# Performance work log

Measured on AMD Instinct MI355X. Metric: run time of the kernel, lower is better.

Reference implementation:

```python
import jax, jax.numpy as jnp
import numpy as np

COORD_W, EDGE_W, COUNT_W, REG_W, CONTRA_W = 1.0, 2.0, 0.1, 0.001, 0.1
MARGIN = 1.0


def setup_inputs() -> dict:
    key = jax.random.key(0)
    ks = jax.random.split(key, 6)
    B, N, D, C = 16, 1024, 128, 2
    return {
        "predicted_coords": jax.random.normal(ks[0], (B, N, C), jnp.float32),
        "points": jax.random.normal(ks[1], (B, N, C), jnp.float32),
        "adjacency_logits": jax.random.normal(ks[2], (B, N, N), jnp.float32),
        "adjacency": jax.random.bernoulli(ks[3], 0.1, (B, N, N)).astype(jnp.float32),
        "node_masks": jnp.ones((B, N), jnp.float32),  # all nodes valid -> n_actual = N
        "predicted_count": jax.random.normal(ks[4], (B, 1), jnp.float32),
        "node_features": jax.random.normal(ks[5], (B, N, D), jnp.float32),
    }


def _bce_with_logits(logits, targets):
    # mean-reduced, numerically stable (matches F.binary_cross_entropy_with_logits)
    return jnp.mean(jnp.maximum(logits, 0.0) - logits * targets
                    + jnp.log1p(jnp.exp(-jnp.abs(logits))))


def _smooth_l1(pred, target):
    d = jnp.abs(pred - target)
    return jnp.mean(jnp.where(d < 1.0, 0.5 * d * d, d - 0.5))


def _contrastive_sample(features, adj):
    # features: [N, D], adj: [N, N]. torch.cdist pairwise euclidean via gram trick.
    nrm = jnp.sum(features * features, axis=-1)              # [N]
    sq = jnp.maximum(nrm[:, None] + nrm[None, :]
                     - 2.0 * (features @ features.T), 0.0)   # [N, N] squared dists
    n = features.shape[0]
    eye = jnp.eye(n, dtype=bool)
    pos_mask = adj > 0.5
    neg_mask = (adj <= 0.5) & (~eye)
    # positive term: mean of distances**2 over positive pairs == mean squared dist
    pos = jnp.sum(jnp.where(pos_mask, sq, 0.0)) / jnp.maximum(jnp.sum(pos_mask), 1)
    dist = jnp.sqrt(jnp.maximum(sq, 1e-12))
    hinge = jnp.square(jax.nn.relu(MARGIN - dist))
    neg = jnp.sum(jnp.where(neg_mask, hinge, 0.0)) / jnp.maximum(jnp.sum(neg_mask), 1)
    return pos + neg


def reference(predicted_coords, points, adjacency_logits, adjacency,
              node_masks, predicted_count, node_features):
    # node_masks are all ones, so the per-sample [:n_actual] slicing is the
    # full tensor; per-sample MSE/BCE means averaged over batch equal global means.
    coord_loss = jnp.mean(jnp.square(predicted_coords - points))
    edge_loss = _bce_with_logits(adjacency_logits, adjacency)
    actual_counts = jnp.sum(node_masks, axis=1)              # [B]
    count_loss = _smooth_l1(predicted_count[:, 0], actual_counts)
    reg_loss = jnp.mean(jnp.square(node_features))
    # contrastive path uses targets['adjacency'] (no predicted_adjacency key)
    contra_loss = jnp.mean(jax.vmap(_contrastive_sample)(node_features, adjacency))
    total = (COORD_W * coord_loss + EDGE_W * edge_loss + COUNT_W * count_loss
             + REG_W * reg_loss + CONTRA_W * contra_loss)
    return total, coord_loss, edge_loss, count_loss, reg_loss, contra_loss
```

## Files before the change

kernel.cpp:

```cpp
#include <hip/hip_runtime.h>
#include <hip/hip_bf16.h>

#define NN 1024
#define DD 128
#define TS 64
#define PITCH 136

#define WS_COORD 0
#define WS_REG   1
#define WS_BCE   2
#define WS_POSN  3
#define WS_POSC  19
#define WS_NEGS  35
#define WS_PDIAG 51
#define WS_CROSS 67
#define WS_CNT   83
#define WS_NORM  112

typedef __bf16 bf16_t;
typedef bf16_t bf16x8 __attribute__((ext_vector_type(8)));
typedef float  f32x4  __attribute__((ext_vector_type(4)));

__device__ __forceinline__ void gload16(const void* g, void* l) {
  __builtin_amdgcn_global_load_lds(
      (const __attribute__((address_space(1))) uint32_t*)g,
      (__attribute__((address_space(3))) uint32_t*)l,
      16, 0, 0);
}

__global__ __launch_bounds__(256) void prep(
    const float* __restrict__ feat, const float* __restrict__ pcoord,
    const float* __restrict__ pts,  const float* __restrict__ masks,
    float* __restrict__ ws) {
  __shared__ float red[4][3];
  const int bx = blockIdx.x;
  const int b = bx >> 3, slab = bx & 7;
  const int t = threadIdx.x, lane = t & 63, w = t >> 6;
  const int sub = lane >> 4, lq = lane & 15;
  const float* fb = feat + (size_t)b * NN * DD;

  float reg = 0.f;
  #pragma unroll
  for (int it = 0; it < 8; ++it) {
    const int node = slab * 128 + it * 16 + w * 4 + sub;
    const float4* src = (const float4*)(fb + (size_t)node * DD) + lq * 2;
    float4 u = src[0], v = src[1];
    float s = u.x*u.x + u.y*u.y + u.z*u.z + u.w*u.w
            + v.x*v.x + v.y*v.y + v.z*v.z + v.w*v.w;
    s += __shfl_xor(s, 1); s += __shfl_xor(s, 2);
    s += __shfl_xor(s, 4); s += __shfl_xor(s, 8);
    if (lq == 0) { ws[WS_NORM + b * NN + node] = s; reg += s; }
  }
  const int ci = bx * 256 + t;
  const float d = pcoord[ci] - pts[ci];
  float coord = d * d;
  float cnt = (t < 128) ? masks[b * NN + slab * 128 + t] : 0.f;

  #pragma unroll
  for (int o = 32; o; o >>= 1) {
    coord += __shfl_xor(coord, o);
    reg   += __shfl_xor(reg, o);
    cnt   += __shfl_xor(cnt, o);
  }
  if (lane == 0) { red[w][0] = coord; red[w][1] = reg; red[w][2] = cnt; }
  __syncthreads();
  if (t == 0) {
    float c = 0.f, r = 0.f, n = 0.f;
    for (int i = 0; i < 4; ++i) { c += red[i][0]; r += red[i][1]; n += red[i][2]; }
    atomicAdd(&ws[WS_COORD], c);
    atomicAdd(&ws[WS_REG], r);
    atomicAdd(&ws[WS_CNT + b], n);
  }
}

__global__ __launch_bounds__(256, 4) void lds_stream(
    const float* __restrict__ logits, const float* __restrict__ adj,
    float* __restrict__ ws) {
  __shared__ __align__(16) float4 sL[2][512];
  __shared__ __align__(16) float4 sA[2][512];
  __shared__ float red[4][4];
  const int bx = blockIdx.x;
  const int b = bx >> 6, rb = bx & 63;
  const int t = threadIdx.x, lane = t & 63, w = t >> 6;
  const float4* Lg = (const float4*)logits + (size_t)b * 262144 + (size_t)rb * 4096;
  const float4* Ag = (const float4*)adj    + (size_t)b * 262144 + (size_t)rb * 4096;
  const float* nrm = ws + WS_NORM + b * NN;

  const float4 nj = ((const float4*)nrm)[t];
  float ni[16];
  #pragma unroll
  for (int k = 0; k < 16; ++k) ni[k] = nrm[rb * 16 + k];

#define STAGE(s) do {                                              \
    gload16(Lg + (s) * 512 + t,       &sL[(s) & 1][t]);            \
    gload16(Lg + (s) * 512 + 256 + t, &sL[(s) & 1][t + 256]);      \
    gload16(Ag + (s) * 512 + t,       &sA[(s) & 1][t]);            \
    gload16(Ag + (s) * 512 + 256 + t, &sA[(s) & 1][t + 256]);      \
  } while (0)

#define ELEM4(L, A, nv, grow) do {                                            \
    bce += fmaxf(L.x, 0.f) - L.x * A.x + __logf(1.f + __expf(-fabsf(L.x)));   \
    bce += fmaxf(L.y, 0.f) - L.y * A.y + __logf(1.f + __expf(-fabsf(L.y)));   \
    bce += fmaxf(L.z, 0.f) - L.z * A.z + __logf(1.f + __expf(-fabsf(L.z)));   \
    bce += fmaxf(L.w, 0.f) - L.w * A.w + __logf(1.f + __expf(-fabsf(L.w)));   \
    const float px = (A.x > 0.5f) ? 1.f : 0.f;                                \
    const float py = (A.y > 0.5f) ? 1.f : 0.f;                                \
    const float pz = (A.z > 0.5f) ? 1.f : 0.f;                                \
    const float pw = (A.w > 0.5f) ? 1.f : 0.f;                                \
    posc += px + py + pz + pw;                                                \
    posn += px * (nv + nj.x) + py * (nv + nj.y)                               \
          + pz * (nv + nj.z) + pw * (nv + nj.w);                              \
    if (((grow) >> 2) == t) {                                                 \
      const int e = (grow) & 3;                                               \
      const float av = (e == 0) ? A.x : (e == 1) ? A.y : (e == 2) ? A.z : A.w;\
      pdiag += (av > 0.5f) ? 1.f : 0.f;                                       \
    } } while (0)

  float bce = 0.f, posc = 0.f, posn = 0.f, pdiag = 0.f;
  STAGE(0);
  #pragma unroll
  for (int s = 0; s < 8; ++s) {
    if (s < 7) STAGE(s + 1);
    const float4 L0 = sL[s & 1][t];
    const float4 A0 = sA[s & 1][t];
    const float4 L1 = sL[s & 1][t + 256];
    const float4 A1 = sA[s & 1][t + 256];
    const int g0 = rb * 16 + s * 2;
    ELEM4(L0, A0, ni[s * 2], g0);
    ELEM4(L1, A1, ni[s * 2 + 1], g0 + 1);
  }
#undef STAGE
#undef ELEM4

  #pragma unroll
  for (int o = 32; o; o >>= 1) {
    bce   += __shfl_xor(bce, o);
    posc  += __shfl_xor(posc, o);
    posn  += __shfl_xor(posn, o);
    pdiag += __shfl_xor(pdiag, o);
  }
  if (lane == 0) {
    red[w][0] = bce; red[w][1] = posc; red[w][2] = posn; red[w][3] = pdiag;
  }
  __syncthreads();
  if (t == 0) {
    float s0 = 0.f, s1 = 0.f, s2 = 0.f, s3 = 0.f;
    for (int i = 0; i < 4; ++i) {
      s0 += red[i][0]; s1 += red[i][1]; s2 += red[i][2]; s3 += red[i][3];
    }
    atomicAdd(&ws[WS_BCE], s0);
    atomicAdd(&ws[WS_POSC + b], s1);
    atomicAdd(&ws[WS_POSN + b], s2);
    atomicAdd(&ws[WS_PDIAG + b], s3);
  }
}

__global__ __launch_bounds__(256, 4) void gram_tiles(
    const float* __restrict__ adj, const float* __restrict__ feat,
    float* __restrict__ ws) {
  __shared__ __align__(16) char smem[2 * TS * PITCH * sizeof(bf16_t)];
  __shared__ float red[4][2];
  bf16_t* lsA = (bf16_t*)smem;
  bf16_t* lsB = (bf16_t*)(smem + TS * PITCH * sizeof(bf16_t));

  const int gid = blockIdx.x;
  const int bm = ((gid & 7) << 9) | (gid >> 3);
  const int b = bm >> 8, tid = bm & 255;
  const int ti = (tid >> 4) << 6, tj = (tid & 15) << 6;
  const int t = threadIdx.x, lane = t & 63, wave = t >> 6;
  const int lrow = lane & 15, quad = lane >> 4;
  const float* fb = feat + (size_t)b * NN * DD;
  const float* nrm = ws + WS_NORM + b * NN;

  const int rbase = wave * 16 + quad * 4;
  const int grow0 = ti + rbase;
  const float* ap = adj + (size_t)b * NN * NN + (size_t)grow0 * NN + (tj + lrow);
  float Af[4][4];
  #pragma unroll
  for (int r = 0; r < 4; ++r)
    #pragma unroll
    for (int fc = 0; fc < 4; ++fc)
      Af[fc][r] = ap[(size_t)r * NN + fc * 16];
  const float4 niv = *(const float4*)(nrm + grow0);
  float njv[4];
  #pragma unroll
  for (int fc = 0; fc < 4; ++fc) njv[fc] = nrm[tj + fc * 16 + lrow];
  __builtin_amdgcn_sched_barrier(0);

  #pragma unroll
  for (int it = 0; it < 8; ++it) {
    const int cid = it * 256 + t;
    const int tile = cid >> 10;
    const int sub = cid & 1023;
    const int row = sub >> 4;
    const int c8 = sub & 15;
    const float* src = fb + (size_t)((tile ? tj : ti) + row) * DD + c8 * 8;
    const float4 u = *(const float4*)src;
    const float4 v = *(const float4*)(src + 4);
    bf16x8 pk;
    pk[0]=(bf16_t)u.x; pk[1]=(bf16_t)u.y; pk[2]=(bf16_t)u.z; pk[3]=(bf16_t)u.w;
    pk[4]=(bf16_t)v.x; pk[5]=(bf16_t)v.y; pk[6]=(bf16_t)v.z; pk[7]=(bf16_t)v.w;
    *(bf16x8*)((tile ? lsB : lsA) + row * PITCH + c8 * 8) = pk;
  }
  __syncthreads();

  f32x4 acc[4];
  #pragma unroll
  for (int fc = 0; fc < 4; ++fc) acc[fc] = (f32x4){0.f, 0.f, 0.f, 0.f};
  #pragma unroll
  for (int k0 = 0; k0 < DD; k0 += 32) {
    const int kc = k0 + quad * 8;
    const bf16x8 aF = *(const bf16x8*)&lsA[(wave * 16 + lrow) * PITCH + kc];
    #pragma unroll
    for (int fc = 0; fc < 4; ++fc) {
      const bf16x8 bF = *(const bf16x8*)&lsB[(fc * 16 + lrow) * PITCH + kc];
      acc[fc] = __builtin_amdgcn_mfma_f32_16x16x32_bf16(aF, bF, acc[fc], 0, 0, 0);
    }
  }

  float cross = 0.f, negs = 0.f;
  #pragma unroll
  for (int fc = 0; fc < 4; ++fc) {
    const int gcol = tj + fc * 16 + lrow;
    #pragma unroll
    for (int r = 0; r < 4; ++r) {
      const float a = Af[fc][r];
      const float g = acc[fc][r];
      if (a > 0.5f) {
        cross += g;
      } else {
        const int grow = grow0 + r;
        const float ni = (r == 0) ? niv.x : (r == 1) ? niv.y : (r == 2) ? niv.z : niv.w;
        const float sq = ni + njv[fc] - 2.f * g;
        if (sq < 1.f && grow != gcol) {
          const float dd = sqrtf(fmaxf(sq, 1e-12f));
          const float h = 1.f - dd;
          negs += h * h;
        }
      }
    }
  }
  #pragma unroll
  for (int o = 32; o; o >>= 1) {
    cross += __shfl_xor(cross, o);
    negs  += __shfl_xor(negs, o);
  }
  if (lane == 0) { red[wave][0] = cross; red[wave][1] = negs; }
  __syncthreads();
  if (t == 0) {
    float s0 = 0.f, s1 = 0.f;
    for (int i = 0; i < 4; ++i) { s0 += red[i][0]; s1 += red[i][1]; }
    atomicAdd(&ws[WS_CROSS + b], s0);
    atomicAdd(&ws[WS_NEGS + b], s1);
  }
}

__global__ void finalize(const float* __restrict__ ws, const float* __restrict__ pcount,
                         float* __restrict__ out) {
  if (threadIdx.x != 0 || blockIdx.x != 0) return;
  const float coord = ws[WS_COORD] / 32768.f;
  const float reg   = ws[WS_REG] / 2097152.f;
  const float edge  = ws[WS_BCE] / 16777216.f;
  float cntl = 0.f, contra = 0.f;
  for (int b = 0; b < 16; ++b) {
    const float d = fabsf(pcount[b] - ws[WS_CNT + b]);
    cntl += (d < 1.f) ? 0.5f * d * d : d - 0.5f;
    const float posc = ws[WS_POSC + b];
    const float pos = (ws[WS_POSN + b] - 2.f * ws[WS_CROSS + b]) / fmaxf(posc, 1.f);
    const float negc = 1024.f * 1024.f - 1024.f - (posc - ws[WS_PDIAG + b]);
    const float neg = ws[WS_NEGS + b] / fmaxf(negc, 1.f);
    contra += pos + neg;
  }
  cntl *= (1.f / 16.f);
  contra *= (1.f / 16.f);
  const float total = coord + 2.f * edge + 0.1f * cntl + 0.001f * reg + 0.1f * contra;
  out[0] = total; out[1] = coord; out[2] = edge;
  out[3] = cntl;  out[4] = reg;   out[5] = contra;
}

extern "C" void kernel_launch(void* const* d_in, const int* in_sizes, int n_in,
                              void* d_out, int out_size, void* d_ws, size_t ws_size,
                              hipStream_t stream) {
  (void)in_sizes; (void)n_in; (void)out_size; (void)ws_size;
  const float* pcoord = (const float*)d_in[0];
  const float* pts    = (const float*)d_in[1];
  const float* logits = (const float*)d_in[2];
  const float* adj    = (const float*)d_in[3];
  const float* masks  = (const float*)d_in[4];
  const float* pcount = (const float*)d_in[5];
  const float* nf     = (const float*)d_in[6];
  float* ws  = (float*)d_ws;
  float* out = (float*)d_out;

  hipMemsetAsync(ws, 0, WS_NORM * sizeof(float), stream);
  prep<<<128, 256, 0, stream>>>(nf, pcoord, pts, masks, ws);
  lds_stream<<<1024, 256, 0, stream>>>(logits, adj, ws);
  gram_tiles<<<4096, 256, 0, stream>>>(adj, nf, ws);
  finalize<<<1, 64, 0, stream>>>(ws, pcount, out);
}
```

Baseline: 242.7 us.

## Restructure gram pass into row bands and interleave stream blocks across batches

The gram kernel now has each block own a 16-row band of one batch. It caches that band's adjacency rows in LDS as bf16 and loops over eight 128-column chunks, converting features to bf16 per chunk, so each block makes one contiguous adjacency pass instead of 64x64 tiles with strided loads. The BCE streaming kernel remaps blocks so each block covers two rows across eight batches, with per-batch partial sums and more atomics per block, which spreads concurrent blocks over different batches. The cost is that the column features are re-read and re-converted by all 64 bands, there are more syncthreads per block, and the block count drops to 1024 blocks of 512 threads, which may reduce latency hiding.

```diff
diff --git a/kernel.cpp b/kernel.cpp
--- a/kernel.cpp
+++ b/kernel.cpp
@@ -3,8 +3,6 @@
 
 #define NN 1024
 #define DD 128
-#define TS 64
-#define PITCH 136
 
 #define WS_COORD 0
 #define WS_REG   1
@@ -18,6 +16,7 @@
 #define WS_NORM  112
 
 typedef __bf16 bf16_t;
+typedef bf16_t bf16x4 __attribute__((ext_vector_type(4)));
 typedef bf16_t bf16x8 __attribute__((ext_vector_type(8)));
 typedef float  f32x4  __attribute__((ext_vector_type(4)));
 
@@ -78,27 +77,28 @@
     float* __restrict__ ws) {
   __shared__ __align__(16) float4 sL[2][512];
   __shared__ __align__(16) float4 sA[2][512];
-  __shared__ float red[4][4];
+  __shared__ float red[4][25];
   const int bx = blockIdx.x;
-  const int b = bx >> 6, rb = bx & 63;
+  const int hi = bx >> 9;
+  const int r0 = (bx & 511) * 2;
   const int t = threadIdx.x, lane = t & 63, w = t >> 6;
-  const float4* Lg = (const float4*)logits + (size_t)b * 262144 + (size_t)rb * 4096;
-  const float4* Ag = (const float4*)adj    + (size_t)b * 262144 + (size_t)rb * 4096;
-  const float* nrm = ws + WS_NORM + b * NN;
-
-  const float4 nj = ((const float4*)nrm)[t];
-  float ni[16];
-  #pragma unroll
-  for (int k = 0; k < 16; ++k) ni[k] = nrm[rb * 16 + k];
-
-#define STAGE(s) do {                                              \
-    gload16(Lg + (s) * 512 + t,       &sL[(s) & 1][t]);            \
-    gload16(Lg + (s) * 512 + 256 + t, &sL[(s) & 1][t + 256]);      \
-    gload16(Ag + (s) * 512 + t,       &sA[(s) & 1][t]);            \
-    gload16(Ag + (s) * 512 + 256 + t, &sA[(s) & 1][t + 256]);      \
+  const float4* Lg = (const float4*)logits;
+  const float4* Ag = (const float4*)adj;
+
+  float bce = 0.f;
+  float pc[8], pn[8], pd[8];
+  #pragma unroll
+  for (int s = 0; s < 8; ++s) { pc[s] = 0.f; pn[s] = 0.f; pd[s] = 0.f; }
+
+#define STAGE(s) do {                                                  \
+    const size_t c4 = (size_t)((s) * 1024 + bx) * 512;                 \
+    gload16(Lg + c4 + t,       &sL[(s) & 1][t]);                       \
+    gload16(Lg + c4 + 256 + t, &sL[(s) & 1][t + 256]);                 \
+    gload16(Ag + c4 + t,       &sA[(s) & 1][t]);                       \
+    gload16(Ag + c4 + 256 + t, &sA[(s) & 1][t + 256]);                 \
   } while (0)
 
-#define ELEM4(L, A, nv, grow) do {                                            \
+#define ELEM4(L, A, nv, grow, S) do {                                         \
     bce += fmaxf(L.x, 0.f) - L.x * A.x + __logf(1.f + __expf(-fabsf(L.x)));   \
     bce += fmaxf(L.y, 0.f) - L.y * A.y + __logf(1.f + __expf(-fabsf(L.y)));   \
     bce += fmaxf(L.z, 0.f) - L.z * A.z + __logf(1.f + __expf(-fabsf(L.z)));   \
@@ -107,149 +107,160 @@
     const float py = (A.y > 0.5f) ? 1.f : 0.f;                                \
     const float pz = (A.z > 0.5f) ? 1.f : 0.f;                                \
     const float pw = (A.w > 0.5f) ? 1.f : 0.f;                                \
-    posc += px + py + pz + pw;                                                \
-    posn += px * (nv + nj.x) + py * (nv + nj.y)                               \
-          + pz * (nv + nj.z) + pw * (nv + nj.w);                              \
+    pc[S] += px + py + pz + pw;                                               \
+    pn[S] += px * (nv + nj.x) + py * (nv + nj.y)                              \
+           + pz * (nv + nj.z) + pw * (nv + nj.w);                             \
     if (((grow) >> 2) == t) {                                                 \
       const int e = (grow) & 3;                                               \
       const float av = (e == 0) ? A.x : (e == 1) ? A.y : (e == 2) ? A.z : A.w;\
-      pdiag += (av > 0.5f) ? 1.f : 0.f;                                       \
+      pd[S] += (av > 0.5f) ? 1.f : 0.f;                                       \
     } } while (0)
 
-  float bce = 0.f, posc = 0.f, posn = 0.f, pdiag = 0.f;
   STAGE(0);
   #pragma unroll
   for (int s = 0; s < 8; ++s) {
     if (s < 7) STAGE(s + 1);
+    const float* nrm_s = ws + WS_NORM + (2 * s + hi) * NN;
+    const float4 nj = ((const float4*)nrm_s)[t];
+    const float ni0 = nrm_s[r0];
+    const float ni1 = nrm_s[r0 + 1];
     const float4 L0 = sL[s & 1][t];
     const float4 A0 = sA[s & 1][t];
     const float4 L1 = sL[s & 1][t + 256];
     const float4 A1 = sA[s & 1][t + 256];
-    const int g0 = rb * 16 + s * 2;
-    ELEM4(L0, A0, ni[s * 2], g0);
-    ELEM4(L1, A1, ni[s * 2 + 1], g0 + 1);
+    ELEM4(L0, A0, ni0, r0, s);
+    ELEM4(L1, A1, ni1, r0 + 1, s);
   }
 #undef STAGE
 #undef ELEM4
 
   #pragma unroll
   for (int o = 32; o; o >>= 1) {
-    bce   += __shfl_xor(bce, o);
-    posc  += __shfl_xor(posc, o);
-    posn  += __shfl_xor(posn, o);
-    pdiag += __shfl_xor(pdiag, o);
+    bce += __shfl_xor(bce, o);
+    #pragma unroll
+    for (int s = 0; s < 8; ++s) {
+      pc[s] += __shfl_xor(pc[s], o);
+      pn[s] += __shfl_xor(pn[s], o);
+      pd[s] += __shfl_xor(pd[s], o);
+    }
   }
   if (lane == 0) {
-    red[w][0] = bce; red[w][1] = posc; red[w][2] = posn; red[w][3] = pdiag;
+    red[w][0] = bce;
+    #pragma unroll
+    for (int s = 0; s < 8; ++s) {
+      red[w][1 + s] = pc[s]; red[w][9 + s] = pn[s]; red[w][17 + s] = pd[s];
+    }
   }
   __syncthreads();
   if (t == 0) {
-    float s0 = 0.f, s1 = 0.f, s2 = 0.f, s3 = 0.f;
-    for (int i = 0; i < 4; ++i) {
-      s0 += red[i][0]; s1 += red[i][1]; s2 += red[i][2]; s3 += red[i][3];
-    }
-    atomicAdd(&ws[WS_BCE], s0);
-    atomicAdd(&ws[WS_POSC + b], s1);
-    atomicAdd(&ws[WS_POSN + b], s2);
-    atomicAdd(&ws[WS_PDIAG + b], s3);
-  }
-}
-
-__global__ __launch_bounds__(256, 4) void gram_tiles(
+    float v[25];
+    for (int i = 0; i < 25; ++i)
+      v[i] = red[0][i] + red[1][i] + red[2][i] + red[3][i];
+    atomicAdd(&ws[WS_BCE], v[0]);
+    for (int s = 0; s < 8; ++s) {
+      const int b = 2 * s + hi;
+      atomicAdd(&ws[WS_POSC + b], v[1 + s]);
+      atomicAdd(&ws[WS_POSN + b], v[9 + s]);
+      atomicAdd(&ws[WS_PDIAG + b], v[17 + s]);
+    }
+  }
+}
+
+__global__ __launch_bounds__(512, 4) void gram_band(
     const float* __restrict__ adj, const float* __restrict__ feat,
     float* __restrict__ ws) {
-  __shared__ __align__(16) char smem[2 * TS * PITCH * sizeof(bf16_t)];
-  __shared__ float red[4][2];
-  bf16_t* lsA = (bf16_t*)smem;
-  bf16_t* lsB = (bf16_t*)(smem + TS * PITCH * sizeof(bf16_t));
-
-  const int gid = blockIdx.x;
-  const int bm = ((gid & 7) << 9) | (gid >> 3);
-  const int b = bm >> 8, tid = bm & 255;
-  const int ti = (tid >> 4) << 6, tj = (tid & 15) << 6;
-  const int t = threadIdx.x, lane = t & 63, wave = t >> 6;
+  __shared__ bf16_t Ab[16][1032];
+  __shared__ bf16_t Fb[16][136];
+  __shared__ bf16_t Fc[128][136];
+  __shared__ float nis[16];
+  __shared__ float red[8][2];
+
+  const int bx = blockIdx.x;
+  const int b = bx >> 6, band = bx & 63;
+  const int t = threadIdx.x, lane = t & 63, w = t >> 6;
   const int lrow = lane & 15, quad = lane >> 4;
   const float* fb = feat + (size_t)b * NN * DD;
   const float* nrm = ws + WS_NORM + b * NN;
 
-  const int rbase = wave * 16 + quad * 4;
-  const int grow0 = ti + rbase;
-  const float* ap = adj + (size_t)b * NN * NN + (size_t)grow0 * NN + (tj + lrow);
-  float Af[4][4];
-  #pragma unroll
-  for (int r = 0; r < 4; ++r)
-    #pragma unroll
-    for (int fc = 0; fc < 4; ++fc)
-      Af[fc][r] = ap[(size_t)r * NN + fc * 16];
-  const float4 niv = *(const float4*)(nrm + grow0);
-  float njv[4];
-  #pragma unroll
-  for (int fc = 0; fc < 4; ++fc) njv[fc] = nrm[tj + fc * 16 + lrow];
-  __builtin_amdgcn_sched_barrier(0);
-
-  #pragma unroll
-  for (int it = 0; it < 8; ++it) {
-    const int cid = it * 256 + t;
-    const int tile = cid >> 10;
-    const int sub = cid & 1023;
-    const int row = sub >> 4;
-    const int c8 = sub & 15;
-    const float* src = fb + (size_t)((tile ? tj : ti) + row) * DD + c8 * 8;
-    const float4 u = *(const float4*)src;
-    const float4 v = *(const float4*)(src + 4);
-    bf16x8 pk;
-    pk[0]=(bf16_t)u.x; pk[1]=(bf16_t)u.y; pk[2]=(bf16_t)u.z; pk[3]=(bf16_t)u.w;
-    pk[4]=(bf16_t)v.x; pk[5]=(bf16_t)v.y; pk[6]=(bf16_t)v.z; pk[7]=(bf16_t)v.w;
-    *(bf16x8*)((tile ? lsB : lsA) + row * PITCH + c8 * 8) = pk;
+  const float4* Abase = (const float4*)(adj + (size_t)b * NN * NN
+                                            + (size_t)band * 16 * NN);
+  float4 Ar[8];
+  #pragma unroll
+  for (int i = 0; i < 8; ++i) Ar[i] = Abase[i * 512 + t];
+
+  {
+    const int row = t >> 5, d4 = t & 31;
+    const float4 v = *(const float4*)(fb + (size_t)(band * 16 + row) * DD + d4 * 4);
+    bf16x4 pk;
+    pk[0] = (bf16_t)v.x; pk[1] = (bf16_t)v.y; pk[2] = (bf16_t)v.z; pk[3] = (bf16_t)v.w;
+    *(bf16x4*)&Fb[row][d4 * 4] = pk;
+  }
+  if (t < 16) nis[t] = nrm[band * 16 + t];
+
+  #pragma unroll
+  for (int i = 0; i < 8; ++i) {
+    const int u = i * 512 + t;
+    const int row = u >> 8, c4 = u & 255;
+    bf16x4 pk;
+    pk[0] = (bf16_t)Ar[i].x; pk[1] = (bf16_t)Ar[i].y;
+    pk[2] = (bf16_t)Ar[i].z; pk[3] = (bf16_t)Ar[i].w;
+    *(bf16x4*)&Ab[row][c4 * 4] = pk;
   }
   __syncthreads();
 
-  f32x4 acc[4];
-  #pragma unroll
-  for (int fc = 0; fc < 4; ++fc) acc[fc] = (f32x4){0.f, 0.f, 0.f, 0.f};
-  #pragma unroll
-  for (int k0 = 0; k0 < DD; k0 += 32) {
-    const int kc = k0 + quad * 8;
-    const bf16x8 aF = *(const bf16x8*)&lsA[(wave * 16 + lrow) * PITCH + kc];
-    #pragma unroll
-    for (int fc = 0; fc < 4; ++fc) {
-      const bf16x8 bF = *(const bf16x8*)&lsB[(fc * 16 + lrow) * PITCH + kc];
-      acc[fc] = __builtin_amdgcn_mfma_f32_16x16x32_bf16(aF, bF, acc[fc], 0, 0, 0);
-    }
-  }
-
   float cross = 0.f, negs = 0.f;
-  #pragma unroll
-  for (int fc = 0; fc < 4; ++fc) {
-    const int gcol = tj + fc * 16 + lrow;
+  for (int cc = 0; cc < 8; ++cc) {
+    #pragma unroll
+    for (int i = 0; i < 8; ++i) {
+      const int u = i * 512 + t;
+      const int node = u >> 5, d4 = u & 31;
+      const float4 v = *(const float4*)(fb + (size_t)(cc * 128 + node) * DD + d4 * 4);
+      bf16x4 pk;
+      pk[0] = (bf16_t)v.x; pk[1] = (bf16_t)v.y; pk[2] = (bf16_t)v.z; pk[3] = (bf16_t)v.w;
+      *(bf16x4*)&Fc[node][d4 * 4] = pk;
+    }
+    __syncthreads();
+
+    f32x4 acc = (f32x4){0.f, 0.f, 0.f, 0.f};
+    #pragma unroll
+    for (int k0 = 0; k0 < DD; k0 += 32) {
+      const int kc = k0 + quad * 8;
+      const bf16x8 aF = *(const bf16x8*)&Fb[lrow][kc];
+      const bf16x8 bF = *(const bf16x8*)&Fc[w * 16 + lrow][kc];
+      acc = __builtin_amdgcn_mfma_f32_16x16x32_bf16(aF, bF, acc, 0, 0, 0);
+    }
+
+    const int gcol = cc * 128 + w * 16 + lrow;
+    const float njv = nrm[gcol];
     #pragma unroll
     for (int r = 0; r < 4; ++r) {
-      const float a = Af[fc][r];
-      const float g = acc[fc][r];
+      const int row = quad * 4 + r;
+      const float g = acc[r];
+      const float a = (float)Ab[row][gcol];
       if (a > 0.5f) {
         cross += g;
       } else {
-        const int grow = grow0 + r;
-        const float ni = (r == 0) ? niv.x : (r == 1) ? niv.y : (r == 2) ? niv.z : niv.w;
-        const float sq = ni + njv[fc] - 2.f * g;
-        if (sq < 1.f && grow != gcol) {
+        const float sq = nis[row] + njv - 2.f * g;
+        if (sq < 1.f && (band * 16 + row) != gcol) {
           const float dd = sqrtf(fmaxf(sq, 1e-12f));
           const float h = 1.f - dd;
           negs += h * h;
         }
       }
     }
-  }
+    __syncthreads();
+  }
+
   #pragma unroll
   for (int o = 32; o; o >>= 1) {
     cross += __shfl_xor(cross, o);
     negs  += __shfl_xor(negs, o);
   }
-  if (lane == 0) { red[wave][0] = cross; red[wave][1] = negs; }
+  if (lane == 0) { red[w][0] = cross; red[w][1] = negs; }
   __syncthreads();
   if (t == 0) {
     float s0 = 0.f, s1 = 0.f;
-    for (int i = 0; i < 4; ++i) { s0 += red[i][0]; s1 += red[i][1]; }
+    for (int i = 0; i < 8; ++i) { s0 += red[i][0]; s1 += red[i][1]; }
     atomicAdd(&ws[WS_CROSS + b], s0);
     atomicAdd(&ws[WS_NEGS + b], s1);
   }
@@ -295,6 +306,6 @@
   hipMemsetAsync(ws, 0, WS_NORM * sizeof(float), stream);
   prep<<<128, 256, 0, stream>>>(nf, pcoord, pts, masks, ws);
   lds_stream<<<1024, 256, 0, stream>>>(logits, adj, ws);
-  gram_tiles<<<4096, 256, 0, stream>>>(adj, nf, ws);
+  gram_band<<<1024, 512, 0, stream>>>(adj, nf, ws);
   finalize<<<1, 64, 0, stream>>>(ws, pcount, out);
 }
```

Measured after the change: 385.6 us. 58.9% more time.
